# Optimization experiments

Measured on AMD Instinct MI355X. Metric: run time of the kernel, lower is better.

The kernel has to match this reference:

```python
import jax, jax.numpy as jnp
import numpy as np

N_POINTS = 50000   # rows of features, also number of output segments
N_EDGES = 1600000  # ragged neighborhood edges (out_idx, in_idx)
CHANNELS = 64


def setup_inputs() -> dict:
    key = jax.random.key(0)
    k1, k2 = jax.random.split(key)
    features = jax.random.normal(k1, (N_POINTS, CHANNELS), dtype=jnp.float32)
    sparse_indices = jax.random.randint(
        k2, (N_EDGES, 2), 0, N_POINTS, dtype=jnp.int64
    )
    return {"features": features, "sparse_indices": sparse_indices}


def reference(features, sparse_indices):
    # sparse_indices[:, 0] = output segment id, sparse_indices[:, 1] = input row.
    out_idx = sparse_indices[:, 0]
    in_idx = sparse_indices[:, 1]
    gathered = features[in_idx]  # [E, C] gather of neighbor features
    # Unsorted segment max over the ragged neighborhoods -> [N, C].
    pooled = jax.ops.segment_max(gathered, out_idx, num_segments=N_POINTS)
    return pooled
```

## Files before the change

kernel.cpp:

```cpp
#include <hip/hip_runtime.h>
#include <hip/hip_bf16.h>
#include <math.h>


#define N_POINTS 50000
#define N_EDGES  1600000
#define CHANNELS 64
#define BIN_SHIFT 6
#define BIN_PTS   64
#define NBINS     782
#define NBINS_PAD 1024
#define CAPB      2560
#define QCAP      2560
#define P1_GRID   256
#define P1_BLK    1024
#define ECHUNK    (N_EDGES / P1_GRID)
#define GCUR_STRIDE 16
#define CVT_TOTAL (N_POINTS * CHANNELS / 4)
#define CVT_PER   ((CVT_TOTAL + P1_GRID - 1) / P1_GRID)

__device__ __forceinline__ unsigned int encode_bf16(float x) {
    unsigned int u = __float_as_uint(x);
    unsigned int r = ((u >> 16) & 1u) + 0x7FFFu;
    unsigned int h = (u + r) >> 16;
    return (h & 0x8000u) ? (h ^ 0xFFFFu) : (h | 0x8000u);
}

__device__ __forceinline__ float decode_u16(unsigned int v) {
    if (v == 0u) return -INFINITY;
    unsigned int h = (v & 0x8000u) ? (v ^ 0x8000u) : (v ^ 0xFFFFu);
    return __uint_as_float(h << 16);
}

__device__ __forceinline__ unsigned int pk_max_u16(unsigned int a, unsigned int b) {
    unsigned int d;
    asm("v_pk_max_u16 %0, %1, %2" : "=v"(d) : "v"(a), "v"(b));
    return d;
}

__global__ __launch_bounds__(P1_BLK) void binsort_cvt_kernel(
    const int2*   __restrict__ idx,
    const float4* __restrict__ feat4,
    uint2*        __restrict__ f16o,
    unsigned int* __restrict__ gcur,
    unsigned int* __restrict__ gstage)
{
    __shared__ unsigned int hist[NBINS_PAD];
    __shared__ unsigned int pfx[NBINS_PAD];
    __shared__ unsigned int gbase[NBINS_PAD];
    __shared__ unsigned int staging[ECHUNK];
    __shared__ unsigned int wsum[16];

    int tid  = threadIdx.x;
    int lane = tid & 63, w = tid >> 6;

    {
        int cb = blockIdx.x * CVT_PER;
        #pragma unroll
        for (int k = 0; k < 4; ++k) {
            int i = cb + k * P1_BLK + tid;
            if (i < cb + CVT_PER && i < CVT_TOTAL) {
                float4 v = feat4[i];
                uint2 r;
                r.x = encode_bf16(v.x) | (encode_bf16(v.y) << 16);
                r.y = encode_bf16(v.z) | (encode_bf16(v.w) << 16);
                f16o[i] = r;
            }
        }
    }

    int base = blockIdx.x * ECHUNK;

    hist[tid] = 0u;
    __syncthreads();

    int2 e[7]; unsigned int slot[7];
    #pragma unroll
    for (int j = 0; j < 7; ++j) {
        int i = j * P1_BLK + tid;
        if (i < ECHUNK) {
            e[j] = idx[base + i];
            slot[j] = atomicAdd(&hist[(unsigned)e[j].x >> BIN_SHIFT], 1u);
        }
    }
    __syncthreads();

    {
        unsigned int a = hist[tid];
        unsigned int inc = a;
        #pragma unroll
        for (int d = 1; d < 64; d <<= 1) {
            unsigned int v = __shfl_up(inc, d, 64);
            if (lane >= d) inc += v;
        }
        if (lane == 63) wsum[w] = inc;
        __syncthreads();
        unsigned int woff = 0;
        #pragma unroll
        for (int k = 0; k < 16; ++k) if (k < w) woff += wsum[k];
        pfx[tid] = woff + inc - a;
        if (a) gbase[tid] = atomicAdd(&gcur[tid * GCUR_STRIDE], a);
    }
    __syncthreads();

    #pragma unroll
    for (int j = 0; j < 7; ++j) {
        int i = j * P1_BLK + tid;
        if (i < ECHUNK) {
            unsigned int dst = (unsigned)e[j].x, src = (unsigned)e[j].y;
            unsigned int bin = dst >> BIN_SHIFT;
            staging[pfx[bin] + slot[j]] =
                (bin << 22) | ((dst & (BIN_PTS - 1)) << 16) | src;
        }
    }
    __syncthreads();

    for (int i = tid; i < ECHUNK; i += P1_BLK) {
        unsigned int v   = staging[i];
        unsigned int bin = v >> 22;
        unsigned int g   = gbase[bin] + ((unsigned)i - pfx[bin]);
        if (g < CAPB) gstage[(size_t)bin * CAPB + g] = v;
    }
}

__global__ __launch_bounds__(512) void pool_kernel(
    const unsigned int* __restrict__ feat16,
    const unsigned int* __restrict__ gcur,
    const unsigned int* __restrict__ gstage,
    float4* __restrict__ out4)
{
    __shared__ unsigned int sorted[QCAP];
    __shared__ unsigned int hist[64];
    __shared__ unsigned int start[65];
    __shared__ unsigned int cur[64];

    int tid = threadIdx.x;
    int bin = blockIdx.x;

    unsigned int cnt = gcur[bin * GCUR_STRIDE]; if (cnt > CAPB) cnt = CAPB;
    const uint4* list4 = (const uint4*)(gstage + (size_t)bin * CAPB);

    if (tid < 64) hist[tid] = 0u;
    __syncthreads();

    unsigned int e[8]; int ne = 0;
    for (unsigned int b4 = tid; b4 * 4 < cnt; b4 += 512) {
        uint4 v = list4[b4];
        unsigned int bi = b4 * 4;
        unsigned int vv[4] = {v.x, v.y, v.z, v.w};
        #pragma unroll
        for (int k = 0; k < 4; ++k) {
            if (bi + k < cnt && ne < 8) {
                e[ne++] = vv[k];
                atomicAdd(&hist[(vv[k] >> 16) & 63], 1u);
            }
        }
    }
    __syncthreads();

    if (tid < 64) {
        unsigned int h = hist[tid], inc = h;
        #pragma unroll
        for (int d = 1; d < 64; d <<= 1) {
            unsigned int v = __shfl_up(inc, d, 64);
            if (tid >= d) inc += v;
        }
        start[tid] = inc - h; cur[tid] = inc - h;
        if (tid == 63) start[64] = inc;
    }
    __syncthreads();

    for (int j = 0; j < ne; ++j) {
        unsigned int v = e[j];
        unsigned int slot = atomicAdd(&cur[(v >> 16) & 63], 1u);
        if (slot < QCAP) sorted[slot] = (v & 0xFFFFu) << 3;
    }
    __syncthreads();

    const uint4* frow = (const uint4*)feat16;
    int g = tid >> 3, ln = tid & 7;
    unsigned int s0 = start[g], s1 = start[g + 1];
    if (s1 > QCAP) s1 = QCAP;

    unsigned int A0=0,A1=0,A2=0,A3=0, B0=0,B1=0,B2=0,B3=0;
    unsigned int C0=0,C1=0,C2=0,C3=0, D0=0,D1=0,D2=0,D3=0;
    unsigned int i = s0;
    for (; i + 4 <= s1; i += 4) {
        unsigned int r0 = sorted[i+0], r1 = sorted[i+1];
        unsigned int r2 = sorted[i+2], r3 = sorted[i+3];
        uint4 u0 = frow[r0 + ln];
        uint4 u1 = frow[r1 + ln];
        uint4 u2 = frow[r2 + ln];
        uint4 u3 = frow[r3 + ln];
        A0 = pk_max_u16(A0, u0.x); A1 = pk_max_u16(A1, u0.y);
        A2 = pk_max_u16(A2, u0.z); A3 = pk_max_u16(A3, u0.w);
        B0 = pk_max_u16(B0, u1.x); B1 = pk_max_u16(B1, u1.y);
        B2 = pk_max_u16(B2, u1.z); B3 = pk_max_u16(B3, u1.w);
        C0 = pk_max_u16(C0, u2.x); C1 = pk_max_u16(C1, u2.y);
        C2 = pk_max_u16(C2, u2.z); C3 = pk_max_u16(C3, u2.w);
        D0 = pk_max_u16(D0, u3.x); D1 = pk_max_u16(D1, u3.y);
        D2 = pk_max_u16(D2, u3.z); D3 = pk_max_u16(D3, u3.w);
    }
    for (; i < s1; ++i) {
        uint4 u = frow[sorted[i] + ln];
        A0 = pk_max_u16(A0, u.x); A1 = pk_max_u16(A1, u.y);
        A2 = pk_max_u16(A2, u.z); A3 = pk_max_u16(A3, u.w);
    }
    A0 = pk_max_u16(pk_max_u16(A0, B0), pk_max_u16(C0, D0));
    A1 = pk_max_u16(pk_max_u16(A1, B1), pk_max_u16(C1, D1));
    A2 = pk_max_u16(pk_max_u16(A2, B2), pk_max_u16(C2, D2));
    A3 = pk_max_u16(pk_max_u16(A3, B3), pk_max_u16(C3, D3));

    int gp = bin * BIN_PTS + g;
    if (gp < N_POINTS) {
        float4 o0, o1;
        o0.x = decode_u16(A0 & 0xFFFFu); o0.y = decode_u16(A0 >> 16);
        o0.z = decode_u16(A1 & 0xFFFFu); o0.w = decode_u16(A1 >> 16);
        o1.x = decode_u16(A2 & 0xFFFFu); o1.y = decode_u16(A2 >> 16);
        o1.z = decode_u16(A3 & 0xFFFFu); o1.w = decode_u16(A3 >> 16);
        out4[(size_t)gp * 16 + ln * 2 + 0] = o0;
        out4[(size_t)gp * 16 + ln * 2 + 1] = o1;
    }
}

extern "C" void kernel_launch(void* const* d_in, const int* in_sizes, int n_in,
                              void* d_out, int out_size, void* d_ws, size_t ws_size,
                              hipStream_t stream) {
    const float4* feat4 = (const float4*)d_in[0];
    const int2*   idx   = (const int2*)d_in[1];

    size_t off_gcur   = 0;
    size_t off_feat16 = (size_t)NBINS_PAD * GCUR_STRIDE * 4;
    size_t off_gstage = off_feat16 + (size_t)N_POINTS * CHANNELS * 2;
    unsigned int* gcur   = (unsigned int*)((char*)d_ws + off_gcur);
    uint2*        f16o   = (uint2*)((char*)d_ws + off_feat16);
    unsigned int* feat16 = (unsigned int*)((char*)d_ws + off_feat16);
    unsigned int* gstage = (unsigned int*)((char*)d_ws + off_gstage);

    hipMemsetAsync(gcur, 0, off_feat16, stream);
    binsort_cvt_kernel<<<P1_GRID, P1_BLK, 0, stream>>>(idx, feat4, f16o, gcur, gstage);
    pool_kernel<<<NBINS, 512, 0, stream>>>(feat16, gcur, gstage, (float4*)d_out);
}
```

Before: 111.6 us.

## Split pool gather into two source-half passes with barrier and prefetched indices

The pool kernel now sub-buckets each destination's edges by whether the source row falls in the lower or upper half of the feature table. Each block gathers all lower-half sources first, hits a block barrier, then does the upper half, so concurrently running blocks touch a smaller working set of the bf16 feature table and get more cache reuse. The unrolled gather loop also prefetches the next four LDS indices one iteration ahead. The cost is extra histogram bins, two barriers inside the gather loop, and a likely shorter unrolled run per pass.

```diff
diff --git a/kernel.cpp b/kernel.cpp
--- a/kernel.cpp
+++ b/kernel.cpp
@@ -12,6 +12,7 @@
 #define NBINS_PAD 1024
 #define CAPB      2560
 #define QCAP      2560
+#define SRC_HALF  25000
 #define P1_GRID   256
 #define P1_BLK    1024
 #define ECHUNK    (N_EDGES / P1_GRID)
@@ -130,9 +131,9 @@
     float4* __restrict__ out4)
 {
     __shared__ unsigned int sorted[QCAP];
-    __shared__ unsigned int hist[64];
-    __shared__ unsigned int start[65];
-    __shared__ unsigned int cur[64];
+    __shared__ unsigned int hist[128];
+    __shared__ unsigned int start[129];
+    __shared__ unsigned int cur[128];
 
     int tid = threadIdx.x;
     int bin = blockIdx.x;
@@ -140,7 +141,7 @@
     unsigned int cnt = gcur[bin * GCUR_STRIDE]; if (cnt > CAPB) cnt = CAPB;
     const uint4* list4 = (const uint4*)(gstage + (size_t)bin * CAPB);
 
-    if (tid < 64) hist[tid] = 0u;
+    if (tid < 128) hist[tid] = 0u;
     __syncthreads();
 
     unsigned int e[8]; int ne = 0;
@@ -151,61 +152,84 @@
         #pragma unroll
         for (int k = 0; k < 4; ++k) {
             if (bi + k < cnt && ne < 8) {
+                unsigned int dl = (vv[k] >> 16) & 63;
+                unsigned int h  = ((vv[k] & 0xFFFFu) >= SRC_HALF) ? 1u : 0u;
                 e[ne++] = vv[k];
-                atomicAdd(&hist[(vv[k] >> 16) & 63], 1u);
+                atomicAdd(&hist[(dl << 1) | h], 1u);
             }
         }
     }
     __syncthreads();
 
     if (tid < 64) {
-        unsigned int h = hist[tid], inc = h;
+        unsigned int h0 = hist[2 * tid], h1 = hist[2 * tid + 1];
+        unsigned int s = h0 + h1, inc = s;
         #pragma unroll
         for (int d = 1; d < 64; d <<= 1) {
             unsigned int v = __shfl_up(inc, d, 64);
             if (tid >= d) inc += v;
         }
-        start[tid] = inc - h; cur[tid] = inc - h;
-        if (tid == 63) start[64] = inc;
+        unsigned int base = inc - s;
+        start[2 * tid] = base;      start[2 * tid + 1] = base + h0;
+        cur[2 * tid]   = base;      cur[2 * tid + 1]   = base + h0;
+        if (tid == 63) start[128] = inc;
     }
     __syncthreads();
 
     for (int j = 0; j < ne; ++j) {
         unsigned int v = e[j];
-        unsigned int slot = atomicAdd(&cur[(v >> 16) & 63], 1u);
+        unsigned int dl = (v >> 16) & 63;
+        unsigned int h  = ((v & 0xFFFFu) >= SRC_HALF) ? 1u : 0u;
+        unsigned int slot = atomicAdd(&cur[(dl << 1) | h], 1u);
         if (slot < QCAP) sorted[slot] = (v & 0xFFFFu) << 3;
     }
     __syncthreads();
 
     const uint4* frow = (const uint4*)feat16;
     int g = tid >> 3, ln = tid & 7;
-    unsigned int s0 = start[g], s1 = start[g + 1];
-    if (s1 > QCAP) s1 = QCAP;
 
     unsigned int A0=0,A1=0,A2=0,A3=0, B0=0,B1=0,B2=0,B3=0;
     unsigned int C0=0,C1=0,C2=0,C3=0, D0=0,D1=0,D2=0,D3=0;
-    unsigned int i = s0;
-    for (; i + 4 <= s1; i += 4) {
-        unsigned int r0 = sorted[i+0], r1 = sorted[i+1];
-        unsigned int r2 = sorted[i+2], r3 = sorted[i+3];
-        uint4 u0 = frow[r0 + ln];
-        uint4 u1 = frow[r1 + ln];
-        uint4 u2 = frow[r2 + ln];
-        uint4 u3 = frow[r3 + ln];
-        A0 = pk_max_u16(A0, u0.x); A1 = pk_max_u16(A1, u0.y);
-        A2 = pk_max_u16(A2, u0.z); A3 = pk_max_u16(A3, u0.w);
-        B0 = pk_max_u16(B0, u1.x); B1 = pk_max_u16(B1, u1.y);
-        B2 = pk_max_u16(B2, u1.z); B3 = pk_max_u16(B3, u1.w);
-        C0 = pk_max_u16(C0, u2.x); C1 = pk_max_u16(C1, u2.y);
-        C2 = pk_max_u16(C2, u2.z); C3 = pk_max_u16(C3, u2.w);
-        D0 = pk_max_u16(D0, u3.x); D1 = pk_max_u16(D1, u3.y);
-        D2 = pk_max_u16(D2, u3.z); D3 = pk_max_u16(D3, u3.w);
-    }
-    for (; i < s1; ++i) {
-        uint4 u = frow[sorted[i] + ln];
-        A0 = pk_max_u16(A0, u.x); A1 = pk_max_u16(A1, u.y);
-        A2 = pk_max_u16(A2, u.z); A3 = pk_max_u16(A3, u.w);
-    }
+
+    for (int pass = 0; pass < 2; ++pass) {
+        unsigned int s0 = start[2 * g + pass], s1 = start[2 * g + pass + 1];
+        if (s1 > QCAP) s1 = QCAP;
+        unsigned int i = s0;
+        if (i + 4 <= s1) {
+            unsigned int n0 = sorted[i+0], n1 = sorted[i+1];
+            unsigned int n2 = sorted[i+2], n3 = sorted[i+3];
+            for (; i + 4 <= s1; ) {
+                unsigned int r0 = n0, r1 = n1, r2 = n2, r3 = n3;
+                unsigned int ip = i + 4;
+                unsigned int lim = s1 - 1;
+                unsigned int j0 = ip + 0 < s1 ? ip + 0 : lim;
+                unsigned int j1 = ip + 1 < s1 ? ip + 1 : lim;
+                unsigned int j2 = ip + 2 < s1 ? ip + 2 : lim;
+                unsigned int j3 = ip + 3 < s1 ? ip + 3 : lim;
+                n0 = sorted[j0]; n1 = sorted[j1]; n2 = sorted[j2]; n3 = sorted[j3];
+                uint4 u0 = frow[r0 + ln];
+                uint4 u1 = frow[r1 + ln];
+                uint4 u2 = frow[r2 + ln];
+                uint4 u3 = frow[r3 + ln];
+                A0 = pk_max_u16(A0, u0.x); A1 = pk_max_u16(A1, u0.y);
+                A2 = pk_max_u16(A2, u0.z); A3 = pk_max_u16(A3, u0.w);
+                B0 = pk_max_u16(B0, u1.x); B1 = pk_max_u16(B1, u1.y);
+                B2 = pk_max_u16(B2, u1.z); B3 = pk_max_u16(B3, u1.w);
+                C0 = pk_max_u16(C0, u2.x); C1 = pk_max_u16(C1, u2.y);
+                C2 = pk_max_u16(C2, u2.z); C3 = pk_max_u16(C3, u2.w);
+                D0 = pk_max_u16(D0, u3.x); D1 = pk_max_u16(D1, u3.y);
+                D2 = pk_max_u16(D2, u3.z); D3 = pk_max_u16(D3, u3.w);
+                i = ip;
+            }
+        }
+        for (; i < s1; ++i) {
+            uint4 u = frow[sorted[i] + ln];
+            A0 = pk_max_u16(A0, u.x); A1 = pk_max_u16(A1, u.y);
+            A2 = pk_max_u16(A2, u.z); A3 = pk_max_u16(A3, u.w);
+        }
+        __syncthreads();
+    }
+
     A0 = pk_max_u16(pk_max_u16(A0, B0), pk_max_u16(C0, D0));
     A1 = pk_max_u16(pk_max_u16(A1, B1), pk_max_u16(C1, D1));
     A2 = pk_max_u16(pk_max_u16(A2, B2), pk_max_u16(C2, D2));
@@ -239,5 +263,5 @@
 
     hipMemsetAsync(gcur, 0, off_feat16, stream);
     binsort_cvt_kernel<<<P1_GRID, P1_BLK, 0, stream>>>(idx, feat4, f16o, gcur, gstage);
-    pool_kernel<<<NBINS, 512, 0, stream>>>(feat16, gcur, gstage, (float4*)d_out);
-}
+    pool_kernel<<<NBINS, 512, 0, stream>>>(feat16, gcur, gstage, (float2*)d_out != nullptr ? (float4*)d_out : (float4*)d_out);
+}
```

After: 112.0 us. Within noise of the previous version (+0.4%).

## Write per-chunk sorted edges contiguously and gather bin segments in pool kernel

Applied to the files above, without the earlier changes.

The binning kernel no longer uses global atomics to reserve space per bin and no longer scatters edges into per-bin global buckets. Each block now writes its locally bin-sorted chunk contiguously with vectorized stores, along with its per-bin prefix offsets. The pool kernel scans those offsets across all chunks and gathers its bin's segments into shared memory. This also removes the memset and the global atomics, and makes the first kernel's stores coalesced. In exchange, every pool block issues 256 small, scattered segment reads.

```diff
diff --git a/kernel.cpp b/kernel.cpp
--- a/kernel.cpp
+++ b/kernel.cpp
@@ -10,12 +10,12 @@
 #define BIN_PTS   64
 #define NBINS     782
 #define NBINS_PAD 1024
-#define CAPB      2560
+#define CAPL      2560
 #define QCAP      2560
 #define P1_GRID   256
 #define P1_BLK    1024
 #define ECHUNK    (N_EDGES / P1_GRID)
-#define GCUR_STRIDE 16
+#define ECHUNK_PAD 6256
 #define CVT_TOTAL (N_POINTS * CHANNELS / 4)
 #define CVT_PER   ((CVT_TOTAL + P1_GRID - 1) / P1_GRID)
 
@@ -42,13 +42,12 @@
     const int2*   __restrict__ idx,
     const float4* __restrict__ feat4,
     uint2*        __restrict__ f16o,
-    unsigned int* __restrict__ gcur,
-    unsigned int* __restrict__ gstage)
+    unsigned int* __restrict__ chunkd,
+    unsigned int* __restrict__ pfxg)
 {
     __shared__ unsigned int hist[NBINS_PAD];
     __shared__ unsigned int pfx[NBINS_PAD];
-    __shared__ unsigned int gbase[NBINS_PAD];
-    __shared__ unsigned int staging[ECHUNK];
+    __shared__ __align__(16) unsigned int staging[ECHUNK_PAD];
     __shared__ unsigned int wsum[16];
 
     int tid  = threadIdx.x;
@@ -99,7 +98,6 @@
         #pragma unroll
         for (int k = 0; k < 16; ++k) if (k < w) woff += wsum[k];
         pfx[tid] = woff + inc - a;
-        if (a) gbase[tid] = atomicAdd(&gcur[tid * GCUR_STRIDE], a);
     }
     __syncthreads();
 
@@ -113,65 +111,100 @@
                 (bin << 22) | ((dst & (BIN_PTS - 1)) << 16) | src;
         }
     }
-    __syncthreads();
-
-    for (int i = tid; i < ECHUNK; i += P1_BLK) {
-        unsigned int v   = staging[i];
-        unsigned int bin = v >> 22;
-        unsigned int g   = gbase[bin] + ((unsigned)i - pfx[bin]);
-        if (g < CAPB) gstage[(size_t)bin * CAPB + g] = v;
+    if (tid < ECHUNK_PAD - ECHUNK) staging[ECHUNK + tid] = 0u;
+    __syncthreads();
+
+    {
+        const uint4* st4 = (const uint4*)staging;
+        uint4* cd4 = (uint4*)(chunkd + (size_t)blockIdx.x * ECHUNK_PAD);
+        #pragma unroll
+        for (int k = 0; k < 2; ++k) {
+            int i = k * P1_BLK + tid;
+            if (i < ECHUNK_PAD / 4) cd4[i] = st4[i];
+        }
+        pfxg[blockIdx.x * NBINS_PAD + tid] = pfx[tid];
     }
 }
 
 __global__ __launch_bounds__(512) void pool_kernel(
     const unsigned int* __restrict__ feat16,
-    const unsigned int* __restrict__ gcur,
-    const unsigned int* __restrict__ gstage,
+    const unsigned int* __restrict__ chunkd,
+    const unsigned int* __restrict__ pfxg,
     float4* __restrict__ out4)
 {
+    __shared__ unsigned int list[CAPL];
     __shared__ unsigned int sorted[QCAP];
+    __shared__ unsigned int choff[P1_GRID];
     __shared__ unsigned int hist[64];
     __shared__ unsigned int start[65];
     __shared__ unsigned int cur[64];
+    __shared__ unsigned int wsum4[4];
+    __shared__ unsigned int Tsh;
 
     int tid = threadIdx.x;
     int bin = blockIdx.x;
-
-    unsigned int cnt = gcur[bin * GCUR_STRIDE]; if (cnt > CAPB) cnt = CAPB;
-    const uint4* list4 = (const uint4*)(gstage + (size_t)bin * CAPB);
+    int lane = tid & 63, w = tid >> 6;
 
     if (tid < 64) hist[tid] = 0u;
-    __syncthreads();
-
-    unsigned int e[8]; int ne = 0;
-    for (unsigned int b4 = tid; b4 * 4 < cnt; b4 += 512) {
-        uint4 v = list4[b4];
-        unsigned int bi = b4 * 4;
-        unsigned int vv[4] = {v.x, v.y, v.z, v.w};
-        #pragma unroll
-        for (int k = 0; k < 4; ++k) {
-            if (bi + k < cnt && ne < 8) {
-                e[ne++] = vv[k];
-                atomicAdd(&hist[(vv[k] >> 16) & 63], 1u);
-            }
-        }
-    }
-    __syncthreads();
-
-    if (tid < 64) {
-        unsigned int h = hist[tid], inc = h;
+
+    unsigned int cntc = 0, segs = 0, inc = 0;
+    if (tid < P1_GRID) {
+        unsigned int s = pfxg[tid * NBINS_PAD + bin];
+        unsigned int e = pfxg[tid * NBINS_PAD + bin + 1];
+        segs = s; cntc = e - s;
+        inc = cntc;
         #pragma unroll
         for (int d = 1; d < 64; d <<= 1) {
             unsigned int v = __shfl_up(inc, d, 64);
-            if (tid >= d) inc += v;
-        }
-        start[tid] = inc - h; cur[tid] = inc - h;
-        if (tid == 63) start[64] = inc;
-    }
-    __syncthreads();
-
-    for (int j = 0; j < ne; ++j) {
-        unsigned int v = e[j];
+            if (lane >= d) inc += v;
+        }
+        if (lane == 63) wsum4[w] = inc;
+    }
+    __syncthreads();
+    if (tid < P1_GRID) {
+        unsigned int woff = 0;
+        #pragma unroll
+        for (int k = 0; k < 4; ++k) if (k < w) woff += wsum4[k];
+        unsigned int off = woff + inc - cntc;
+        choff[tid] = off;
+        if (tid == P1_GRID - 1) Tsh = off + cntc;
+    }
+    __syncthreads();
+
+    unsigned int T = Tsh; if (T > CAPL) T = CAPL;
+
+    {
+        int c = tid >> 1, h = tid & 1;
+        unsigned int s = pfxg[c * NBINS_PAD + bin];
+        unsigned int e = pfxg[c * NBINS_PAD + bin + 1];
+        unsigned int n = e - s;
+        unsigned int off = choff[c];
+        unsigned int g0 = (unsigned)c * ECHUNK_PAD + s;
+        for (unsigned int j = h; j < n; j += 2) {
+            unsigned int v = chunkd[g0 + j];
+            if (off + j < CAPL) list[off + j] = v;
+        }
+    }
+    __syncthreads();
+
+    for (unsigned int t = tid; t < T; t += 512)
+        atomicAdd(&hist[(list[t] >> 16) & 63], 1u);
+    __syncthreads();
+
+    if (tid < 64) {
+        unsigned int h = hist[tid], inc2 = h;
+        #pragma unroll
+        for (int d = 1; d < 64; d <<= 1) {
+            unsigned int v = __shfl_up(inc2, d, 64);
+            if (tid >= d) inc2 += v;
+        }
+        start[tid] = inc2 - h; cur[tid] = inc2 - h;
+        if (tid == 63) start[64] = inc2;
+    }
+    __syncthreads();
+
+    for (unsigned int t = tid; t < T; t += 512) {
+        unsigned int v = list[t];
         unsigned int slot = atomicAdd(&cur[(v >> 16) & 63], 1u);
         if (slot < QCAP) sorted[slot] = (v & 0xFFFFu) << 3;
     }
@@ -229,15 +262,14 @@
     const float4* feat4 = (const float4*)d_in[0];
     const int2*   idx   = (const int2*)d_in[1];
 
-    size_t off_gcur   = 0;
-    size_t off_feat16 = (size_t)NBINS_PAD * GCUR_STRIDE * 4;
-    size_t off_gstage = off_feat16 + (size_t)N_POINTS * CHANNELS * 2;
-    unsigned int* gcur   = (unsigned int*)((char*)d_ws + off_gcur);
+    size_t off_feat16 = 0;
+    size_t off_chunk  = (size_t)N_POINTS * CHANNELS * 2;
+    size_t off_pfxg   = off_chunk + (size_t)P1_GRID * ECHUNK_PAD * 4;
     uint2*        f16o   = (uint2*)((char*)d_ws + off_feat16);
     unsigned int* feat16 = (unsigned int*)((char*)d_ws + off_feat16);
-    unsigned int* gstage = (unsigned int*)((char*)d_ws + off_gstage);
-
-    hipMemsetAsync(gcur, 0, off_feat16, stream);
-    binsort_cvt_kernel<<<P1_GRID, P1_BLK, 0, stream>>>(idx, feat4, f16o, gcur, gstage);
-    pool_kernel<<<NBINS, 512, 0, stream>>>(feat16, gcur, gstage, (float4*)d_out);
-}
+    unsigned int* chunkd = (unsigned int*)((char*)d_ws + off_chunk);
+    unsigned int* pfxg   = (unsigned int*)((char*)d_ws + off_pfxg);
+
+    binsort_cvt_kernel<<<P1_GRID, P1_BLK, 0, stream>>>(idx, feat4, f16o, chunkd, pfxg);
+    pool_kernel<<<NBINS, 512, 0, stream>>>(feat16, chunkd, pfxg, (float4*)d_out);
+}
```

New measurement: 104.6 us. -6.2%, faster.
